# Optimization experiments

Hardware: AMD Instinct MI355X
Metric: run time of the kernel (lower is better)

## Reference

```python
import jax, jax.numpy as jnp
import numpy as np

N_NODES = 100000
N_CHANNELS = 64
N_EDGES = 1200000
K_CHEB = 6


def _cheb_norm(edge_index, num_nodes):
    # PyG ChebConv sym normalization with lambda_max=2.0:
    # L_hat = 2L/lambda_max - I = -D^{-1/2} A D^{-1/2} (diagonal becomes 0)
    row, col = edge_index[0], edge_index[1]
    ones = jnp.ones(edge_index.shape[1], dtype=jnp.float32)
    deg = jax.ops.segment_sum(ones, row, num_segments=num_nodes)
    dinv = jnp.where(deg > 0, jax.lax.rsqrt(jnp.where(deg > 0, deg, 1.0)), 0.0)
    norm = -dinv[row] * dinv[col]  # [E]
    return norm


def _propagate(x, row, col, norm, num_nodes):
    # out[i] = sum_{e: row[e]==i} norm[e] * x[col[e]]
    msgs = norm[:, None] * x[col]  # [E, C]
    return jax.ops.segment_sum(msgs, row, num_segments=num_nodes)


def _cheb_conv(x, W, b, row, col, norm, num_nodes):
    # W: [K, C_in, C_out]; Chebyshev recursion T0=x, T1=Lhat x, Tk=2 Lhat T_{k-1}-T_{k-2}
    Tx0 = x
    out = Tx0 @ W[0]
    Tx1 = _propagate(Tx0, row, col, norm, num_nodes)
    out = out + Tx1 @ W[1]
    for k in range(2, W.shape[0]):
        Tx2 = 2.0 * _propagate(Tx1, row, col, norm, num_nodes) - Tx0
        out = out + Tx2 @ W[k]
        Tx0, Tx1 = Tx1, Tx2
    return out + b


def setup_inputs() -> dict:
    key = jax.random.key(0)
    ks = jax.random.split(key, 8)
    pos = jax.random.normal(ks[0], (N_NODES, N_CHANNELS), dtype=jnp.float32)
    edge_index = jax.random.randint(ks[1], (2, N_EDGES), 0, N_NODES, dtype=jnp.int64)
    scale = 1.0 / np.sqrt(N_CHANNELS)
    W1 = jax.random.normal(ks[2], (K_CHEB, N_CHANNELS, N_CHANNELS), dtype=jnp.float32) * scale
    W2 = jax.random.normal(ks[3], (K_CHEB, N_CHANNELS, N_CHANNELS), dtype=jnp.float32) * scale
    W3 = jax.random.normal(ks[4], (K_CHEB, N_CHANNELS, N_CHANNELS), dtype=jnp.float32) * scale
    b1 = jnp.zeros((N_CHANNELS,), dtype=jnp.float32)
    b2 = jnp.zeros((N_CHANNELS,), dtype=jnp.float32)
    b3 = jnp.zeros((N_CHANNELS,), dtype=jnp.float32)
    return {"pos": pos, "edge_index": edge_index,
            "W1": W1, "b1": b1, "W2": W2, "b2": b2, "W3": W3, "b3": b3}


def reference(pos, edge_index, W1, b1, W2, b2, W3, b3):
    num_nodes = pos.shape[0]
    row, col = edge_index[0], edge_index[1]
    norm = _cheb_norm(edge_index, num_nodes)
    residual = pos
    h = jax.nn.relu(_cheb_conv(pos, W1, b1, row, col, norm, num_nodes))
    h = jax.nn.relu(_cheb_conv(h, W2, b2, row, col, norm, num_nodes))
    h = jax.nn.relu(_cheb_conv(h, W3, b3, row, col, norm, num_nodes))
    return h + residual
```

## Files before the change

### kernel.cpp

```cpp
#include <hip/hip_runtime.h>
#include <hip/hip_bf16.h>
#include <math.h>

#define NN 100000
#define NE 1200000
#define NC 64
#define NB 391
#define NTILE 6250

typedef unsigned short u16;
typedef __attribute__((ext_vector_type(8))) short short8;
typedef __attribute__((ext_vector_type(4))) float f32x4;

__device__ __forceinline__ float bf2f(u16 u) {
    return __uint_as_float(((unsigned)u) << 16);
}
__device__ __forceinline__ u16 f2bf(float f) {
    __hip_bfloat16 h = __float2bfloat16(f);
    return *reinterpret_cast<u16*>(&h);
}

__global__ __launch_bounds__(256) void deg_kernel(const int* __restrict__ ei, int* __restrict__ deg) {
    int e = blockIdx.x * 256 + threadIdx.x;
    if (e < NE) atomicAdd(&deg[ei[e]], 1);
}

__global__ __launch_bounds__(256) void scan1_kernel(const int* __restrict__ deg,
                                                    int* __restrict__ tmp,
                                                    int* __restrict__ bsum) {
    __shared__ int s[256];
    int i = blockIdx.x * 256 + threadIdx.x;
    int v = (i < NN) ? deg[i] : 0;
    s[threadIdx.x] = v;
    __syncthreads();
    for (int off = 1; off < 256; off <<= 1) {
        int t = (threadIdx.x >= off) ? s[threadIdx.x - off] : 0;
        __syncthreads();
        s[threadIdx.x] += t;
        __syncthreads();
    }
    if (i < NN) tmp[i] = s[threadIdx.x];
    if (threadIdx.x == 255) bsum[blockIdx.x] = s[255];
}

__global__ __launch_bounds__(512) void scan2_kernel(const int* __restrict__ bsum,
                                                    int* __restrict__ boff) {
    __shared__ int s[512];
    int t = threadIdx.x;
    int v = (t < NB) ? bsum[t] : 0;
    s[t] = v;
    __syncthreads();
    for (int off = 1; off < 512; off <<= 1) {
        int u = (t >= off) ? s[t - off] : 0;
        __syncthreads();
        s[t] += u;
        __syncthreads();
    }
    if (t < NB) boff[t] = s[t] - v;
}

__global__ __launch_bounds__(256) void scan3_kernel(const int* __restrict__ deg,
                                                    const int* __restrict__ tmp,
                                                    const int* __restrict__ boff,
                                                    int* __restrict__ row_ptr,
                                                    float* __restrict__ dinv) {
    int i = blockIdx.x * 256 + threadIdx.x;
    if (i >= NN) return;
    int d = deg[i];
    int start = tmp[i] - d + boff[blockIdx.x];
    row_ptr[i] = start;
    dinv[i] = (d > 0) ? rsqrtf((float)d) : 0.f;
    if (i == NN - 1) row_ptr[NN] = start + d;
}

__global__ __launch_bounds__(256) void fill_kernel(const int* __restrict__ ei,
                                                   const int* __restrict__ row_ptr,
                                                   int* __restrict__ cnt,
                                                   const float* __restrict__ dinv,
                                                   int2* __restrict__ csr) {
    int e = blockIdx.x * 256 + threadIdx.x;
    if (e >= NE) return;
    int r = ei[e];
    int c = ei[NE + e];
    int p = atomicAdd(&cnt[r], 1);
    csr[row_ptr[r] + p] = make_int2(c, (int)__float_as_uint(dinv[c]));
}

__global__ __launch_bounds__(256) void wcat_kernel(const float* __restrict__ W1,
                                                   const float* __restrict__ W2,
                                                   const float* __restrict__ W3,
                                                   u16* __restrict__ WT) {
    int idx = blockIdx.x * 256 + threadIdx.x;
    if (idx >= 3 * 64 * 384) return;
    int l = idx / (64 * 384);
    int rem = idx - l * (64 * 384);
    int co = rem / 384;
    int kk = rem - co * 384;
    const float* W = (l == 0) ? W1 : ((l == 1) ? W2 : W3);
    WT[idx] = f2bf(W[kk * 64 + co]);
}

__global__ __launch_bounds__(256) void cvt_kernel(const float4* __restrict__ in,
                                                  ushort4* __restrict__ outb, int n4) {
    int i = blockIdx.x * 256 + threadIdx.x;
    if (i < n4) {
        float4 v = in[i];
        ushort4 u;
        u.x = f2bf(v.x); u.y = f2bf(v.y); u.z = f2bf(v.z); u.w = f2bf(v.w);
        outb[i] = u;
    }
}

template <bool FIRST>
__global__ __launch_bounds__(256, 6) void prop_kernel(
    const u16* __restrict__ t0, const u16* __restrict__ t1, u16* __restrict__ t2,
    const int2* __restrict__ csr, const int* __restrict__ row_ptr,
    const float* __restrict__ dinv) {
    int lane = threadIdx.x & 63;
    int wid = __builtin_amdgcn_readfirstlane((int)(threadIdx.x >> 6));
    int base = (blockIdx.x * 4 + wid) * 4;

    int sN[4], dN[4];
    int2 ce[4];
#pragma unroll
    for (int n = 0; n < 4; ++n) {
        int i = base + n;
        sN[n] = row_ptr[i];
        dN[n] = row_ptr[i + 1] - sN[n];
        ce[n] = make_int2(0, 0);
        if (dN[n] > 0) ce[n] = csr[sN[n] + min(lane, dN[n] - 1)];
    }

    float dv[4], x0[4];
#pragma unroll
    for (int n = 0; n < 4; ++n) {
        dv[n] = dinv[base + n];
        x0[n] = 0.f;
        if (!FIRST) x0[n] = bf2f(t0[(size_t)(base + n) * 64 + lane]);
    }

    int kmax = max(max(min(dN[0], 64), min(dN[1], 64)),
                   max(min(dN[2], 64), min(dN[3], 64)));

    float acc[4] = {0.f, 0.f, 0.f, 0.f};
#pragma unroll 4
    for (int k = 0; k < kmax; ++k) {
#pragma unroll
        for (int n = 0; n < 4; ++n) {
            int col = __builtin_amdgcn_readlane(ce[n].x, k);
            float w = __uint_as_float((unsigned)__builtin_amdgcn_readlane(ce[n].y, k));
            w = (k < dN[n]) ? w : 0.f;
            acc[n] = fmaf(w, bf2f(t1[(size_t)col * 64 + lane]), acc[n]);
        }
    }

#pragma unroll
    for (int n = 0; n < 4; ++n) {
        for (int b = 64; b < dN[n]; b += 64) {
            int rem = min(dN[n] - b, 64);
            int2 c2 = csr[sN[n] + b + min(lane, rem - 1)];
            for (int k = 0; k < rem; ++k) {
                int col = __builtin_amdgcn_readlane(c2.x, k);
                float w = __uint_as_float((unsigned)__builtin_amdgcn_readlane(c2.y, k));
                acc[n] = fmaf(w, bf2f(t1[(size_t)col * 64 + lane]), acc[n]);
            }
        }
    }

#pragma unroll
    for (int n = 0; n < 4; ++n) {
        float p = -dv[n] * acc[n];
        float v = FIRST ? p : fmaf(2.f, p, -x0[n]);
        t2[(size_t)(base + n) * 64 + lane] = f2bf(v);
    }
}

template <int MODE>
__global__ __launch_bounds__(256) void gemm_kernel(
    const u16* __restrict__ T0, const u16* __restrict__ T1, const u16* __restrict__ T2,
    const u16* __restrict__ T3, const u16* __restrict__ T4, const u16* __restrict__ T5,
    const u16* __restrict__ WT, const float* __restrict__ bias,
    u16* __restrict__ xout, float* __restrict__ fout, const float* __restrict__ pos) {
    int lane = threadIdx.x & 63;
    int wid = __builtin_amdgcn_readfirstlane((int)(threadIdx.x >> 6));
    int tile = blockIdx.x * 4 + wid;
    if (tile >= NTILE) return;
    int r = lane & 15;
    int kg = lane >> 4;
    int arow = tile * 16 + r;

    f32x4 acc[4];
#pragma unroll
    for (int t = 0; t < 4; ++t) {
        float b = bias[t * 16 + r];
        acc[t] = (f32x4){b, b, b, b};
    }

    const u16* Ts[6] = {T0, T1, T2, T3, T4, T5};
#pragma unroll
    for (int kb = 0; kb < 6; ++kb) {
        const u16* Tb = Ts[kb];
        short8 a0 = *(const short8*)(Tb + (size_t)arow * 64 + kg * 8);
        short8 a1 = *(const short8*)(Tb + (size_t)arow * 64 + 32 + kg * 8);
#pragma unroll
        for (int t = 0; t < 4; ++t) {
            const u16* wb = WT + (size_t)(t * 16 + r) * 384 + kb * 64 + kg * 8;
            short8 b0 = *(const short8*)(wb);
            short8 b1 = *(const short8*)(wb + 32);
            acc[t] = __builtin_amdgcn_mfma_f32_16x16x32_bf16(a0, b0, acc[t], 0, 0, 0);
            acc[t] = __builtin_amdgcn_mfma_f32_16x16x32_bf16(a1, b1, acc[t], 0, 0, 0);
        }
    }

#pragma unroll
    for (int t = 0; t < 4; ++t) {
#pragma unroll
        for (int rr = 0; rr < 4; ++rr) {
            int row = tile * 16 + kg * 4 + rr;
            int col = t * 16 + r;
            float v = acc[t][rr];
            if (MODE == 0) {
                xout[(size_t)row * 64 + col] = f2bf(fmaxf(v, 0.f));
            } else {
                fout[(size_t)row * 64 + col] = fmaxf(v, 0.f) + pos[(size_t)row * 64 + col];
            }
        }
    }
}

extern "C" void kernel_launch(void* const* d_in, const int* in_sizes, int n_in,
                              void* d_out, int out_size, void* d_ws, size_t ws_size,
                              hipStream_t stream) {
    const float* pos = (const float*)d_in[0];
    const int* ei = (const int*)d_in[1];
    const float* W1 = (const float*)d_in[2];
    const float* b1 = (const float*)d_in[3];
    const float* W2 = (const float*)d_in[4];
    const float* b2 = (const float*)d_in[5];
    const float* W3 = (const float*)d_in[6];
    const float* b3 = (const float*)d_in[7];
    float* out = (float*)d_out;

    char* ws = (char*)d_ws;
    size_t off = 0;
    auto alloc = [&](size_t bytes) {
        void* p = ws + off;
        off += (bytes + 1023) & ~(size_t)1023;
        return p;
    };
    int* deg = (int*)alloc(NN * 4);
    float* dinv = (float*)alloc(NN * 4);
    int* row_ptr = (int*)alloc((NN + 1) * 4);
    int* cnt = (int*)alloc(NN * 4);
    int* tmp = (int*)alloc(NN * 4);
    int* bsum = (int*)alloc(NB * 4);
    int* boff = (int*)alloc(NB * 4);
    int2* csr = (int2*)alloc((size_t)NE * 8);
    u16* WT = (u16*)alloc((size_t)3 * 64 * 384 * 2);
    u16* X = (u16*)alloc((size_t)NN * NC * 2);
    u16* T1 = (u16*)alloc((size_t)NN * NC * 2);
    u16* T2 = (u16*)alloc((size_t)NN * NC * 2);
    u16* T3 = (u16*)alloc((size_t)NN * NC * 2);
    u16* T4 = (u16*)alloc((size_t)NN * NC * 2);
    u16* T5 = (u16*)alloc((size_t)NN * NC * 2);

    hipMemsetAsync(deg, 0, NN * 4, stream);
    hipMemsetAsync(cnt, 0, NN * 4, stream);
    deg_kernel<<<(NE + 255) / 256, 256, 0, stream>>>(ei, deg);
    scan1_kernel<<<NB, 256, 0, stream>>>(deg, tmp, bsum);
    scan2_kernel<<<1, 512, 0, stream>>>(bsum, boff);
    scan3_kernel<<<NB, 256, 0, stream>>>(deg, tmp, boff, row_ptr, dinv);
    fill_kernel<<<(NE + 255) / 256, 256, 0, stream>>>(ei, row_ptr, cnt, dinv, csr);
    wcat_kernel<<<(3 * 64 * 384 + 255) / 256, 256, 0, stream>>>(W1, W2, W3, WT);

    const int G = NN / 16;
    const int G4 = (NN * NC / 4) / 256;
    const int GG = (NTILE + 3) / 4;

    cvt_kernel<<<G4, 256, 0, stream>>>((const float4*)pos, (ushort4*)X, NN * NC / 4);

    prop_kernel<true><<<G, 256, 0, stream>>>(X, X, T1, csr, row_ptr, dinv);
    prop_kernel<false><<<G, 256, 0, stream>>>(X, T1, T2, csr, row_ptr, dinv);
    prop_kernel<false><<<G, 256, 0, stream>>>(T1, T2, T3, csr, row_ptr, dinv);
    prop_kernel<false><<<G, 256, 0, stream>>>(T2, T3, T4, csr, row_ptr, dinv);
    prop_kernel<false><<<G, 256, 0, stream>>>(T3, T4, T5, csr, row_ptr, dinv);
    gemm_kernel<0><<<GG, 256, 0, stream>>>(X, T1, T2, T3, T4, T5, WT, b1, X, nullptr, nullptr);

    prop_kernel<true><<<G, 256, 0, stream>>>(X, X, T1, csr, row_ptr, dinv);
    prop_kernel<false><<<G, 256, 0, stream>>>(X, T1, T2, csr, row_ptr, dinv);
    prop_kernel<false><<<G, 256, 0, stream>>>(T1, T2, T3, csr, row_ptr, dinv);
    prop_kernel<false><<<G, 256, 0, stream>>>(T2, T3, T4, csr, row_ptr, dinv);
    prop_kernel<false><<<G, 256, 0, stream>>>(T3, T4, T5, csr, row_ptr, dinv);
    gemm_kernel<0><<<GG, 256, 0, stream>>>(X, T1, T2, T3, T4, T5, WT + 24576, b2, X, nullptr, nullptr);

    prop_kernel<true><<<G, 256, 0, stream>>>(X, X, T1, csr, row_ptr, dinv);
    prop_kernel<false><<<G, 256, 0, stream>>>(X, T1, T2, csr, row_ptr, dinv);
    prop_kernel<false><<<G, 256, 0, stream>>>(T1, T2, T3, csr, row_ptr, dinv);
    prop_kernel<false><<<G, 256, 0, stream>>>(T2, T3, T4, csr, row_ptr, dinv);
    prop_kernel<false><<<G, 256, 0, stream>>>(T3, T4, T5, csr, row_ptr, dinv);
    gemm_kernel<1><<<GG, 256, 0, stream>>>(X, T1, T2, T3, T4, T5, WT + 2 * 24576, b3, nullptr, out, pos);
}
```

Baseline: 894.5 us.

## Vectorize SpMM gathers, stage GEMM weights in LDS, reuse atomic slot positions

The propagation kernel now has each quarter-wave gather a different neighbour with 8-byte vector loads covering four channels, so four edges are processed per iteration, and reduces the partial sums with cross-lane shuffles before a packed store. The GEMM kernel copies the weight slice into padded shared memory and computes two 16-row tiles per wave so each B fragment is reused. CSR construction keeps the slot returned by the degree atomic, which removes the second atomic pass and the counter memset at the cost of an extra per-edge buffer. The trade-off is more shuffles and extra work for padded edges in the propagation kernel, plus shared-memory pressure in the GEMM.

```diff
diff --git a/kernel.cpp b/kernel.cpp
--- a/kernel.cpp
+++ b/kernel.cpp
@@ -7,22 +7,26 @@
 #define NC 64
 #define NB 391
 #define NTILE 6250
+#define NT2 3125
+#define WSTRIDE 392
 
 typedef unsigned short u16;
+typedef unsigned int u32;
 typedef __attribute__((ext_vector_type(8))) short short8;
 typedef __attribute__((ext_vector_type(4))) float f32x4;
 
-__device__ __forceinline__ float bf2f(u16 u) {
-    return __uint_as_float(((unsigned)u) << 16);
-}
+__device__ __forceinline__ float bflo(u32 u) { return __uint_as_float(u << 16); }
+__device__ __forceinline__ float bfhi(u32 u) { return __uint_as_float(u & 0xffff0000u); }
 __device__ __forceinline__ u16 f2bf(float f) {
     __hip_bfloat16 h = __float2bfloat16(f);
     return *reinterpret_cast<u16*>(&h);
 }
 
-__global__ __launch_bounds__(256) void deg_kernel(const int* __restrict__ ei, int* __restrict__ deg) {
+__global__ __launch_bounds__(256) void deg_kernel(const int* __restrict__ ei,
+                                                  int* __restrict__ deg,
+                                                  int* __restrict__ ppos) {
     int e = blockIdx.x * 256 + threadIdx.x;
-    if (e < NE) atomicAdd(&deg[ei[e]], 1);
+    if (e < NE) ppos[e] = atomicAdd(&deg[ei[e]], 1);
 }
 
 __global__ __launch_bounds__(256) void scan1_kernel(const int* __restrict__ deg,
@@ -75,15 +79,14 @@
 
 __global__ __launch_bounds__(256) void fill_kernel(const int* __restrict__ ei,
                                                    const int* __restrict__ row_ptr,
-                                                   int* __restrict__ cnt,
+                                                   const int* __restrict__ ppos,
                                                    const float* __restrict__ dinv,
                                                    int2* __restrict__ csr) {
     int e = blockIdx.x * 256 + threadIdx.x;
     if (e >= NE) return;
     int r = ei[e];
     int c = ei[NE + e];
-    int p = atomicAdd(&cnt[r], 1);
-    csr[row_ptr[r] + p] = make_int2(c, (int)__float_as_uint(dinv[c]));
+    csr[row_ptr[r] + ppos[e]] = make_int2(c, (int)__float_as_uint(dinv[c]));
 }
 
 __global__ __launch_bounds__(256) void wcat_kernel(const float* __restrict__ W1,
@@ -119,6 +122,8 @@
     int lane = threadIdx.x & 63;
     int wid = __builtin_amdgcn_readfirstlane((int)(threadIdx.x >> 6));
     int base = (blockIdx.x * 4 + wid) * 4;
+    int q = lane >> 4;
+    int c4 = lane & 15;
 
     int sN[4], dN[4];
     int2 ce[4];
@@ -131,26 +136,39 @@
         if (dN[n] > 0) ce[n] = csr[sN[n] + min(lane, dN[n] - 1)];
     }
 
-    float dv[4], x0[4];
+    float dv[4];
+    uint2 x0u[4];
 #pragma unroll
     for (int n = 0; n < 4; ++n) {
         dv[n] = dinv[base + n];
-        x0[n] = 0.f;
-        if (!FIRST) x0[n] = bf2f(t0[(size_t)(base + n) * 64 + lane]);
+        x0u[n] = make_uint2(0u, 0u);
+        if (!FIRST) x0u[n] = *(const uint2*)(t0 + (size_t)(base + n) * 64 + c4 * 4);
     }
 
     int kmax = max(max(min(dN[0], 64), min(dN[1], 64)),
                    max(min(dN[2], 64), min(dN[3], 64)));
 
-    float acc[4] = {0.f, 0.f, 0.f, 0.f};
-#pragma unroll 4
-    for (int k = 0; k < kmax; ++k) {
+    float acc[4][4] = {{0.f}};
+#pragma unroll 2
+    for (int k = 0; k < kmax; k += 4) {
 #pragma unroll
         for (int n = 0; n < 4; ++n) {
-            int col = __builtin_amdgcn_readlane(ce[n].x, k);
-            float w = __uint_as_float((unsigned)__builtin_amdgcn_readlane(ce[n].y, k));
-            w = (k < dN[n]) ? w : 0.f;
-            acc[n] = fmaf(w, bf2f(t1[(size_t)col * 64 + lane]), acc[n]);
+            int c0 = __builtin_amdgcn_readlane(ce[n].x, k);
+            int c1 = __builtin_amdgcn_readlane(ce[n].x, k + 1);
+            int c2 = __builtin_amdgcn_readlane(ce[n].x, k + 2);
+            int c3 = __builtin_amdgcn_readlane(ce[n].x, k + 3);
+            float w0 = __uint_as_float((u32)__builtin_amdgcn_readlane(ce[n].y, k));
+            float w1 = __uint_as_float((u32)__builtin_amdgcn_readlane(ce[n].y, k + 1));
+            float w2 = __uint_as_float((u32)__builtin_amdgcn_readlane(ce[n].y, k + 2));
+            float w3 = __uint_as_float((u32)__builtin_amdgcn_readlane(ce[n].y, k + 3));
+            int col = (q & 2) ? ((q & 1) ? c3 : c2) : ((q & 1) ? c1 : c0);
+            float w = (q & 2) ? ((q & 1) ? w3 : w2) : ((q & 1) ? w1 : w0);
+            w = ((k + q) < dN[n]) ? w : 0.f;
+            uint2 v = *(const uint2*)(t1 + (size_t)col * 64 + c4 * 4);
+            acc[n][0] = fmaf(w, bflo(v.x), acc[n][0]);
+            acc[n][1] = fmaf(w, bfhi(v.x), acc[n][1]);
+            acc[n][2] = fmaf(w, bflo(v.y), acc[n][2]);
+            acc[n][3] = fmaf(w, bfhi(v.y), acc[n][3]);
         }
     }
 
@@ -158,20 +176,53 @@
     for (int n = 0; n < 4; ++n) {
         for (int b = 64; b < dN[n]; b += 64) {
             int rem = min(dN[n] - b, 64);
-            int2 c2 = csr[sN[n] + b + min(lane, rem - 1)];
-            for (int k = 0; k < rem; ++k) {
-                int col = __builtin_amdgcn_readlane(c2.x, k);
-                float w = __uint_as_float((unsigned)__builtin_amdgcn_readlane(c2.y, k));
-                acc[n] = fmaf(w, bf2f(t1[(size_t)col * 64 + lane]), acc[n]);
+            int2 c2e = csr[sN[n] + b + min(lane, rem - 1)];
+            for (int k = 0; k < rem; k += 4) {
+                int cc[4];
+                float ww[4];
+#pragma unroll
+                for (int j = 0; j < 4; ++j) {
+                    int idx = min(k + j, 63);
+                    cc[j] = __builtin_amdgcn_readlane(c2e.x, idx);
+                    ww[j] = __uint_as_float((u32)__builtin_amdgcn_readlane(c2e.y, idx));
+                }
+                int col = (q & 2) ? ((q & 1) ? cc[3] : cc[2]) : ((q & 1) ? cc[1] : cc[0]);
+                float w = (q & 2) ? ((q & 1) ? ww[3] : ww[2]) : ((q & 1) ? ww[1] : ww[0]);
+                w = ((k + q) < rem) ? w : 0.f;
+                uint2 v = *(const uint2*)(t1 + (size_t)col * 64 + c4 * 4);
+                acc[n][0] = fmaf(w, bflo(v.x), acc[n][0]);
+                acc[n][1] = fmaf(w, bfhi(v.x), acc[n][1]);
+                acc[n][2] = fmaf(w, bflo(v.y), acc[n][2]);
+                acc[n][3] = fmaf(w, bfhi(v.y), acc[n][3]);
             }
         }
     }
 
 #pragma unroll
     for (int n = 0; n < 4; ++n) {
-        float p = -dv[n] * acc[n];
-        float v = FIRST ? p : fmaf(2.f, p, -x0[n]);
-        t2[(size_t)(base + n) * 64 + lane] = f2bf(v);
+        float s[4];
+#pragma unroll
+        for (int j = 0; j < 4; ++j) {
+            float a = acc[n][j];
+            a += __shfl_xor(a, 16);
+            a += __shfl_xor(a, 32);
+            s[j] = -dv[n] * a;
+        }
+        float v0, v1, v2, v3;
+        if (FIRST) {
+            v0 = s[0]; v1 = s[1]; v2 = s[2]; v3 = s[3];
+        } else {
+            v0 = fmaf(2.f, s[0], -bflo(x0u[n].x));
+            v1 = fmaf(2.f, s[1], -bfhi(x0u[n].x));
+            v2 = fmaf(2.f, s[2], -bflo(x0u[n].y));
+            v3 = fmaf(2.f, s[3], -bfhi(x0u[n].y));
+        }
+        if (q == 0) {
+            uint2 o;
+            o.x = (u32)f2bf(v0) | ((u32)f2bf(v1) << 16);
+            o.y = (u32)f2bf(v2) | ((u32)f2bf(v3) << 16);
+            *(uint2*)(t2 + (size_t)(base + n) * 64 + c4 * 4) = o;
+        }
     }
 }
 
@@ -181,34 +232,48 @@
     const u16* __restrict__ T3, const u16* __restrict__ T4, const u16* __restrict__ T5,
     const u16* __restrict__ WT, const float* __restrict__ bias,
     u16* __restrict__ xout, float* __restrict__ fout, const float* __restrict__ pos) {
+    __shared__ u16 Wl[64 * WSTRIDE];
+    for (int i = threadIdx.x; i < 64 * 192; i += 256) {
+        int co = i / 192;
+        int k2 = i - co * 192;
+        *(u32*)(&Wl[co * WSTRIDE + k2 * 2]) = *(const u32*)(WT + co * 384 + k2 * 2);
+    }
+    __syncthreads();
+
     int lane = threadIdx.x & 63;
     int wid = __builtin_amdgcn_readfirstlane((int)(threadIdx.x >> 6));
-    int tile = blockIdx.x * 4 + wid;
-    if (tile >= NTILE) return;
+    int st = blockIdx.x * 4 + wid;
+    if (st >= NT2) return;
     int r = lane & 15;
     int kg = lane >> 4;
-    int arow = tile * 16 + r;
-
-    f32x4 acc[4];
+    int rowA = st * 32 + r;
+    int rowB = st * 32 + 16 + r;
+
+    f32x4 accA[4], accB[4];
 #pragma unroll
     for (int t = 0; t < 4; ++t) {
         float b = bias[t * 16 + r];
-        acc[t] = (f32x4){b, b, b, b};
+        accA[t] = (f32x4){b, b, b, b};
+        accB[t] = (f32x4){b, b, b, b};
     }
 
     const u16* Ts[6] = {T0, T1, T2, T3, T4, T5};
 #pragma unroll
     for (int kb = 0; kb < 6; ++kb) {
         const u16* Tb = Ts[kb];
-        short8 a0 = *(const short8*)(Tb + (size_t)arow * 64 + kg * 8);
-        short8 a1 = *(const short8*)(Tb + (size_t)arow * 64 + 32 + kg * 8);
+        short8 a0 = *(const short8*)(Tb + (size_t)rowA * 64 + kg * 8);
+        short8 a1 = *(const short8*)(Tb + (size_t)rowA * 64 + 32 + kg * 8);
+        short8 a2 = *(const short8*)(Tb + (size_t)rowB * 64 + kg * 8);
+        short8 a3 = *(const short8*)(Tb + (size_t)rowB * 64 + 32 + kg * 8);
 #pragma unroll
         for (int t = 0; t < 4; ++t) {
-            const u16* wb = WT + (size_t)(t * 16 + r) * 384 + kb * 64 + kg * 8;
+            const u16* wb = &Wl[(t * 16 + r) * WSTRIDE + kb * 64 + kg * 8];
             short8 b0 = *(const short8*)(wb);
             short8 b1 = *(const short8*)(wb + 32);
-            acc[t] = __builtin_amdgcn_mfma_f32_16x16x32_bf16(a0, b0, acc[t], 0, 0, 0);
-            acc[t] = __builtin_amdgcn_mfma_f32_16x16x32_bf16(a1, b1, acc[t], 0, 0, 0);
+            accA[t] = __builtin_amdgcn_mfma_f32_16x16x32_bf16(a0, b0, accA[t], 0, 0, 0);
+            accA[t] = __builtin_amdgcn_mfma_f32_16x16x32_bf16(a1, b1, accA[t], 0, 0, 0);
+            accB[t] = __builtin_amdgcn_mfma_f32_16x16x32_bf16(a2, b0, accB[t], 0, 0, 0);
+            accB[t] = __builtin_amdgcn_mfma_f32_16x16x32_bf16(a3, b1, accB[t], 0, 0, 0);
         }
     }
 
@@ -216,13 +281,17 @@
     for (int t = 0; t < 4; ++t) {
 #pragma unroll
         for (int rr = 0; rr < 4; ++rr) {
-            int row = tile * 16 + kg * 4 + rr;
             int col = t * 16 + r;
-            float v = acc[t][rr];
+            int row0 = st * 32 + kg * 4 + rr;
+            int row1 = row0 + 16;
+            float vA = accA[t][rr];
+            float vB = accB[t][rr];
             if (MODE == 0) {
-                xout[(size_t)row * 64 + col] = f2bf(fmaxf(v, 0.f));
+                xout[(size_t)row0 * 64 + col] = f2bf(fmaxf(vA, 0.f));
+                xout[(size_t)row1 * 64 + col] = f2bf(fmaxf(vB, 0.f));
             } else {
-                fout[(size_t)row * 64 + col] = fmaxf(v, 0.f) + pos[(size_t)row * 64 + col];
+                fout[(size_t)row0 * 64 + col] = fmaxf(vA, 0.f) + pos[(size_t)row0 * 64 + col];
+                fout[(size_t)row1 * 64 + col] = fmaxf(vB, 0.f) + pos[(size_t)row1 * 64 + col];
             }
         }
     }
@@ -251,10 +320,10 @@
     int* deg = (int*)alloc(NN * 4);
     float* dinv = (float*)alloc(NN * 4);
     int* row_ptr = (int*)alloc((NN + 1) * 4);
-    int* cnt = (int*)alloc(NN * 4);
     int* tmp = (int*)alloc(NN * 4);
     int* bsum = (int*)alloc(NB * 4);
     int* boff = (int*)alloc(NB * 4);
+    int* ppos = (int*)alloc((size_t)NE * 4);
     int2* csr = (int2*)alloc((size_t)NE * 8);
     u16* WT = (u16*)alloc((size_t)3 * 64 * 384 * 2);
     u16* X = (u16*)alloc((size_t)NN * NC * 2);
@@ -265,17 +334,16 @@
     u16* T5 = (u16*)alloc((size_t)NN * NC * 2);
 
     hipMemsetAsync(deg, 0, NN * 4, stream);
-    hipMemsetAsync(cnt, 0, NN * 4, stream);
-    deg_kernel<<<(NE + 255) / 256, 256, 0, stream>>>(ei, deg);
+    deg_kernel<<<(NE + 255) / 256, 256, 0, stream>>>(ei, deg, ppos);
     scan1_kernel<<<NB, 256, 0, stream>>>(deg, tmp, bsum);
     scan2_kernel<<<1, 512, 0, stream>>>(bsum, boff);
     scan3_kernel<<<NB, 256, 0, stream>>>(deg, tmp, boff, row_ptr, dinv);
-    fill_kernel<<<(NE + 255) / 256, 256, 0, stream>>>(ei, row_ptr, cnt, dinv, csr);
+    fill_kernel<<<(NE + 255) / 256, 256, 0, stream>>>(ei, row_ptr, ppos, dinv, csr);
     wcat_kernel<<<(3 * 64 * 384 + 255) / 256, 256, 0, stream>>>(W1, W2, W3, WT);
 
     const int G = NN / 16;
     const int G4 = (NN * NC / 4) / 256;
-    const int GG = (NTILE + 3) / 4;
+    const int GG = (NT2 + 3) / 4;
 
     cvt_kernel<<<G4, 256, 0, stream>>>((const float4*)pos, (ushort4*)X, NN * NC / 4);
 
```

Result: faster. 849.0 us (-5.1%).
